# Optimization experiments

Hardware: AMD Instinct MI355X
Metric: run time of the kernel (lower is better)

The kernel has to match this reference:

```python
import jax, jax.numpy as jnp
import numpy as np

N = 50000
E = 800000
NODE_F = 128
LIN = 128
HID = 32
HEADS = 2
OUT = 64
NCLS = 8
NEG_SLOPE = 0.2


def _lin_params(key, fan_in, fan_out, scale=0.05):
    k1, k2 = jax.random.split(key)
    W = jax.random.normal(k1, (fan_in, fan_out), jnp.float32) * scale
    b = jax.random.normal(k2, (fan_out,), jnp.float32) * scale
    return W, b


def setup_inputs() -> dict:
    key = jax.random.key(0)
    ks = jax.random.split(key, 12)
    h = jax.random.normal(ks[0], (N, NODE_F), jnp.float32)
    edge_w = jax.random.uniform(ks[1], (E,), jnp.float32, 1e-3, 1.0)
    src = jax.random.randint(ks[2], (E,), 0, N, jnp.int32)
    dst = jax.random.randint(ks[3], (E,), 0, N, jnp.int32)
    Wn, bn = _lin_params(ks[4], NODE_F, LIN)
    W1s, b1s = _lin_params(ks[5], LIN, HEADS * HID)
    W1d, b1d = _lin_params(ks[6], LIN, HEADS * HID)
    attn1 = jax.random.normal(ks[7], (HEADS, HID), jnp.float32) * 0.05
    W2s, b2s = _lin_params(ks[8], HEADS * HID, OUT)
    W2d, b2d = _lin_params(ks[9], HEADS * HID, OUT)
    attn2 = jax.random.normal(ks[10], (1, OUT), jnp.float32) * 0.05
    k11, k12, k13 = jax.random.split(ks[11], 3)
    Wc1, bc1 = _lin_params(k11, OUT, OUT // 2)
    Wc2, bc2 = _lin_params(k12, OUT // 2, OUT // 4)
    Wcls, bcls = _lin_params(k13, 2 * (OUT // 4), NCLS)
    return dict(h=h, edge_w=edge_w, src=src, dst=dst, Wn=Wn, bn=bn,
                W1s=W1s, b1s=b1s, W1d=W1d, b1d=b1d, attn1=attn1,
                W2s=W2s, b2s=b2s, W2d=W2d, b2d=b2d, attn2=attn2,
                Wc1=Wc1, bc1=bc1, Wc2=Wc2, bc2=bc2, Wcls=Wcls, bcls=bcls)


def _segment_softmax(logits, seg, num_segments):
    # logits: [E, H], seg: [E] destination node ids
    m = jax.ops.segment_max(logits, seg, num_segments=num_segments)
    e = jnp.exp(logits - m[seg])
    s = jax.ops.segment_sum(e, seg, num_segments=num_segments)
    return e / s[seg]


def _gatv2(x, src, dst, Ws, bs, Wd, bd, attn, heads, dim):
    n = x.shape[0]
    fs = (x @ Ws + bs).reshape(n, heads, dim)
    fd = (x @ Wd + bd).reshape(n, heads, dim)
    e = jax.nn.leaky_relu(fs[src] + fd[dst], NEG_SLOPE)  # [E,H,D]
    logits = jnp.einsum('ehd,hd->eh', e, attn)
    alpha = _segment_softmax(logits, dst, n)  # [E,H]
    return jax.ops.segment_sum(fs[src] * alpha[..., None], dst, num_segments=n)


def _forward(h, edge_w, src, dst, Wn, bn, W1s, b1s, W1d, b1d, attn1,
             W2s, b2s, W2d, b2d, attn2, Wc1, bc1, Wc2, bc2, Wcls, bcls):
    n = h.shape[0]
    # EdgeWeightNorm(norm='both'): w / sqrt(out_wdeg(src) * in_wdeg(dst))
    out_wdeg = jax.ops.segment_sum(edge_w, src, num_segments=n)
    in_wdeg = jax.ops.segment_sum(edge_w, dst, num_segments=n)
    norm_w = edge_w * jax.lax.rsqrt(out_wdeg[src]) * jax.lax.rsqrt(in_wdeg[dst])

    node_f = h @ Wn + bn
    # GATv2 layer 1 (dropout is identity in eval)
    g1 = _gatv2(node_f, src, dst, W1s, b1s, W1d, b1d, attn1, HEADS, HID)
    x = jax.nn.elu(g1).reshape(n, HEADS * HID)
    # GATv2 layer 2 (single head)
    g2 = _gatv2(x, src, dst, W2s, b2s, W2d, b2d, attn2, 1, OUT)
    x = jax.nn.elu(g2).reshape(n, OUT)

    # GraphConv norm='none' with edge_weight: sum_in(w * (xW)[src]) + b
    xm = x @ Wc1
    c1 = jax.ops.segment_sum(xm[src] * norm_w[:, None], dst, num_segments=n) + bc1
    x = jax.nn.elu(c1)

    # GraphConv norm='both' (unweighted degrees, clamped to >=1)
    ones_e = jnp.ones((src.shape[0],), x.dtype)
    dout = jnp.clip(jax.ops.segment_sum(ones_e, src, num_segments=n), 1.0)
    din = jnp.clip(jax.ops.segment_sum(ones_e, dst, num_segments=n), 1.0)
    xs = (x @ Wc2) * jax.lax.rsqrt(dout)[:, None]
    c2 = jax.ops.segment_sum(xs[src], dst, num_segments=n) * jax.lax.rsqrt(din)[:, None] + bc2
    x = jax.nn.elu(c2)

    # MLPPredictor: per-edge score from concat(src, dst) features
    score = jnp.concatenate([x[src], x[dst]], axis=1) @ Wcls + bcls
    return score


def reference(h, edge_w, src, dst, Wn, bn, W1s, b1s, W1d, b1d, attn1,
              W2s, b2s, W2d, b2d, attn2, Wc1, bc1, Wc2, bc2, Wcls, bcls):
    return _forward(h, edge_w, src, dst, Wn, bn, W1s, b1s, W1d, b1d, attn1,
                    W2s, b2s, W2d, b2d, attn2, Wc1, bc1, Wc2, bc2, Wcls, bcls)
```

## Files before the change

kernel.cpp:

```cpp
#include <hip/hip_runtime.h>
#include <math.h>

#define NN 50000
#define NE 800000
#define SCAN_BLOCKS ((NN + 255) / 256)

__device__ __forceinline__ float elu1(float x) { return x > 0.f ? x : expm1f(x); }
__device__ __forceinline__ float lrelu(float x) { return x >= 0.f ? x : 0.2f * x; }

__global__ __launch_bounds__(256) void zero_kernel(float* __restrict__ p, int n) {
  int i = blockIdx.x * blockDim.x + threadIdx.x;
  int stride = gridDim.x * blockDim.x;
  for (; i < n; i += stride) p[i] = 0.f;
}

__global__ __launch_bounds__(256) void combine_weights(
    const float* __restrict__ Wn, const float* __restrict__ bn,
    const float* __restrict__ W1s, const float* __restrict__ b1s,
    const float* __restrict__ W1d, const float* __restrict__ b1d,
    float* __restrict__ Wns, float* __restrict__ Wnd,
    float* __restrict__ bns, float* __restrict__ bnd) {
  int t = blockIdx.x * blockDim.x + threadIdx.x;
  if (t < 8192) {
    int i = t >> 6, o = t & 63;
    float acc = 0.f;
    for (int k = 0; k < 128; ++k) acc += Wn[i * 128 + k] * W1s[k * 64 + o];
    Wns[t] = acc;
  } else if (t < 16384) {
    int u = t - 8192;
    int i = u >> 6, o = u & 63;
    float acc = 0.f;
    for (int k = 0; k < 128; ++k) acc += Wn[i * 128 + k] * W1d[k * 64 + o];
    Wnd[u] = acc;
  } else if (t < 16448) {
    int o = t - 16384;
    float acc = b1s[o];
    for (int k = 0; k < 128; ++k) acc += bn[k] * W1s[k * 64 + o];
    bns[o] = acc;
  } else if (t < 16512) {
    int o = t - 16448;
    float acc = b1d[o];
    for (int k = 0; k < 128; ++k) acc += bn[k] * W1d[k * 64 + o];
    bnd[o] = acc;
  }
}

__global__ __launch_bounds__(256) void edge_stats(const float* __restrict__ ew,
                                                  const int* __restrict__ src,
                                                  const int* __restrict__ dst,
                                                  unsigned long long* __restrict__ degw,
                                                  int* __restrict__ cnt) {
  int e = blockIdx.x * blockDim.x + threadIdx.x;
  if (e >= NE) return;
  int s = src[e], d = dst[e];
  unsigned long long pk = (1ULL << 44) | (unsigned long long)(ew[e] * 4294967296.0f);
  atomicAdd(&degw[s], pk);
  atomicAdd(&cnt[d], 1);
}

__global__ __launch_bounds__(256) void decode_degrees(const unsigned long long* __restrict__ degw,
                                                      float* __restrict__ deg) {
  int i = blockIdx.x * blockDim.x + threadIdx.x;
  if (i >= NN) return;
  unsigned long long v = degw[i];
  deg[i] = (float)((double)(v & ((1ULL << 44) - 1)) * (1.0 / 4294967296.0));
  deg[NN + i] = (float)(v >> 44);
}

__global__ __launch_bounds__(256) void csr_block_sums(const int* __restrict__ cnt,
                                                      int* __restrict__ part) {
  __shared__ int sh[256];
  int i = blockIdx.x * 256 + threadIdx.x;
  sh[threadIdx.x] = (i < NN) ? cnt[i] : 0;
  __syncthreads();
  for (int s = 128; s > 0; s >>= 1) {
    if (threadIdx.x < s) sh[threadIdx.x] += sh[threadIdx.x + s];
    __syncthreads();
  }
  if (threadIdx.x == 0) part[blockIdx.x] = sh[0];
}

__global__ __launch_bounds__(256) void csr_scan_part(int* __restrict__ part) {
  __shared__ int sh[256];
  int t = threadIdx.x;
  int v = (t < SCAN_BLOCKS) ? part[t] : 0;
  sh[t] = v;
  __syncthreads();
  for (int off = 1; off < 256; off <<= 1) {
    int add = (t >= off) ? sh[t - off] : 0;
    __syncthreads();
    sh[t] += add;
    __syncthreads();
  }
  if (t < SCAN_BLOCKS) part[t] = sh[t] - v;
}

__global__ __launch_bounds__(256) void csr_scan_write(const int* __restrict__ cnt,
                                                      const int* __restrict__ part,
                                                      int* __restrict__ row_start) {
  __shared__ int sh[256];
  int i = blockIdx.x * 256 + threadIdx.x;
  int t = threadIdx.x;
  int v = (i < NN) ? cnt[i] : 0;
  sh[t] = v;
  __syncthreads();
  for (int off = 1; off < 256; off <<= 1) {
    int add = (t >= off) ? sh[t - off] : 0;
    __syncthreads();
    sh[t] += add;
    __syncthreads();
  }
  if (i < NN) row_start[i] = part[blockIdx.x] + sh[t] - v;
  if (i == 0) row_start[NN] = NE;
}

__global__ __launch_bounds__(256) void csr_fill(const int* __restrict__ src,
                                                const int* __restrict__ dst,
                                                const float* __restrict__ ew,
                                                const int* __restrict__ row_start,
                                                int* __restrict__ fill,
                                                int2* __restrict__ psrcw) {
  int e = blockIdx.x * blockDim.x + threadIdx.x;
  if (e >= NE) return;
  int d = dst[e];
  int pos = row_start[d] + atomicAdd(&fill[d], 1);
  psrcw[pos] = make_int2(src[e], __float_as_int(ew[e]));
}

template <int K, int M, bool ELU_IN, int RS, bool DUAL>
__global__ __launch_bounds__(256) void node_gemm(const float* __restrict__ X,
                                                 const float* __restrict__ W1,
                                                 const float* __restrict__ b1,
                                                 const float* __restrict__ W2,
                                                 const float* __restrict__ b2,
                                                 const float* __restrict__ cnt,
                                                 float* __restrict__ Y1,
                                                 float* __restrict__ Y2) {
  constexpr int RPT = 4;
  constexpr int RG = 256 / M;
  constexpr int ROWS = RG * RPT;
  __shared__ float xs[ROWS][K];
  int row0 = blockIdx.x * ROWS;
  int t = threadIdx.x;
  for (int idx = t; idx < ROWS * K; idx += 256) {
    int r = idx / K, k = idx - r * K;
    int row = row0 + r;
    float v = (row < NN) ? X[row * K + k] : 0.f;
    if (ELU_IN) v = elu1(v);
    xs[r][k] = v;
  }
  __syncthreads();
  int m = t % M, rg = t / M;
  int rbase = rg * RPT;
  float acc1[RPT], acc2[RPT];
#pragma unroll
  for (int j = 0; j < RPT; ++j) {
    acc1[j] = b1 ? b1[m] : 0.f;
    if (DUAL) acc2[j] = b2 ? b2[m] : 0.f;
  }
#pragma unroll 4
  for (int k = 0; k < K; ++k) {
    float w1 = W1[k * M + m];
    float w2 = DUAL ? W2[k * M + m] : 0.f;
#pragma unroll
    for (int j = 0; j < RPT; ++j) {
      float x = xs[rbase + j][k];
      acc1[j] += x * w1;
      if (DUAL) acc2[j] += x * w2;
    }
  }
#pragma unroll
  for (int j = 0; j < RPT; ++j) {
    int row = row0 + rbase + j;
    if (row >= NN) continue;
    float sc = 1.f;
    if (RS == 1) sc = rsqrtf(fmaxf(cnt[row], 1.f));
    if (RS == 2) {
      float wv = cnt[row];
      sc = (wv > 0.f) ? rsqrtf(wv) : 0.f;
    }
    Y1[row * M + m] = acc1[j] * sc;
    if (DUAL) Y2[row * M + m] = acc2[j] * sc;
  }
}

template <int HALFW>
__global__ __launch_bounds__(256) void gat_fused(const int* __restrict__ row_start,
                                                 const int2* __restrict__ psrcw,
                                                 const float* __restrict__ fs,
                                                 const float* __restrict__ fd,
                                                 const float* __restrict__ attn,
                                                 float* __restrict__ g) {
  int n = blockIdx.x * 4 + (threadIdx.x >> 6);
  if (n >= NN) return;
  int lane = threadIdx.x & 63;
  int beg = row_start[n], end = row_start[n + 1];
  float fdv = fd[n * 64 + lane];
  float av = attn[lane];
  float acc = 0.f, den = 0.f;
  int i = beg;
  for (; i + 3 < end; i += 4) {
    int s0 = psrcw[i].x, s1 = psrcw[i + 1].x, s2 = psrcw[i + 2].x, s3 = psrcw[i + 3].x;
    float f0 = fs[s0 * 64 + lane];
    float f1 = fs[s1 * 64 + lane];
    float f2 = fs[s2 * 64 + lane];
    float f3 = fs[s3 * 64 + lane];
    float v0 = lrelu(f0 + fdv) * av;
    float v1 = lrelu(f1 + fdv) * av;
    float v2 = lrelu(f2 + fdv) * av;
    float v3 = lrelu(f3 + fdv) * av;
#pragma unroll
    for (int m = 16; m >= 1; m >>= 1) {
      v0 += __shfl_xor(v0, m, 64);
      v1 += __shfl_xor(v1, m, 64);
      v2 += __shfl_xor(v2, m, 64);
      v3 += __shfl_xor(v3, m, 64);
    }
    if (!HALFW) {
      v0 += __shfl_xor(v0, 32, 64);
      v1 += __shfl_xor(v1, 32, 64);
      v2 += __shfl_xor(v2, 32, 64);
      v3 += __shfl_xor(v3, 32, 64);
    }
    float p0 = __expf(v0);
    float p1 = __expf(v1);
    float p2 = __expf(v2);
    float p3 = __expf(v3);
    acc += f0 * p0 + f1 * p1 + f2 * p2 + f3 * p3;
    den += p0 + p1 + p2 + p3;
  }
  for (; i < end; ++i) {
    int s = psrcw[i].x;
    float fsv = fs[s * 64 + lane];
    float v = lrelu(fsv + fdv) * av;
#pragma unroll
    for (int m = 16; m >= 1; m >>= 1) v += __shfl_xor(v, m, 64);
    if (!HALFW) v += __shfl_xor(v, 32, 64);
    float p = __expf(v);
    acc += fsv * p;
    den += p;
  }
  g[n * 64 + lane] = (end > beg) ? acc / den : 0.f;
}

__global__ __launch_bounds__(256) void gconv1_fused(const int* __restrict__ row_start,
                                                    const int2* __restrict__ psrcw,
                                                    const float* __restrict__ ym,
                                                    const float* __restrict__ bc1,
                                                    float* __restrict__ x3a) {
  int n = blockIdx.x * 4 + (threadIdx.x >> 6);
  if (n >= NN) return;
  int lane = threadIdx.x & 63;
  int half = lane >> 5, f = lane & 31;
  int beg = row_start[n], end = row_start[n + 1];
  float acc = 0.f, wsum = 0.f;
  int i = beg + half;
  for (; i + 2 < end; i += 4) {
    int2 a = psrcw[i], b = psrcw[i + 2];
    float wa = __int_as_float(a.y), wb = __int_as_float(b.y);
    acc += ym[a.x * 32 + f] * wa + ym[b.x * 32 + f] * wb;
    wsum += wa + wb;
  }
  if (i < end) {
    int2 a = psrcw[i];
    float wa = __int_as_float(a.y);
    acc += ym[a.x * 32 + f] * wa;
    wsum += wa;
  }
  acc += __shfl_xor(acc, 32, 64);
  wsum += __shfl_xor(wsum, 32, 64);
  if (lane < 32) {
    float r = (end > beg) ? acc * rsqrtf(wsum) : 0.f;
    x3a[n * 32 + lane] = elu1(r + bc1[lane]);
  }
}

__global__ __launch_bounds__(256) void gconv2_fused(const int* __restrict__ row_start,
                                                    const int2* __restrict__ psrcw,
                                                    const float* __restrict__ xs,
                                                    const float* __restrict__ bc2,
                                                    float* __restrict__ x4) {
  int n = blockIdx.x * 4 + (threadIdx.x >> 6);
  if (n >= NN) return;
  int lane = threadIdx.x & 63;
  int q = lane >> 4, f = lane & 15;
  int beg = row_start[n], end = row_start[n + 1];
  float acc = 0.f;
  int i = beg + q;
  for (; i + 4 < end; i += 8) acc += xs[psrcw[i].x * 16 + f] + xs[psrcw[i + 4].x * 16 + f];
  if (i < end) acc += xs[psrcw[i].x * 16 + f];
  acc += __shfl_xor(acc, 16, 64);
  acc += __shfl_xor(acc, 32, 64);
  if (lane < 16) {
    float len = (float)(end - beg);
    x4[n * 16 + lane] = elu1(acc * rsqrtf(fmaxf(len, 1.f)) + bc2[lane]);
  }
}

__global__ __launch_bounds__(256) void classifier_kernel(const int* __restrict__ src,
                                                         const int* __restrict__ dst,
                                                         const float* __restrict__ x4,
                                                         const float* __restrict__ Wcls,
                                                         const float* __restrict__ bcls,
                                                         float* __restrict__ out) {
  __shared__ float w[256];
  __shared__ float bb[8];
  if (threadIdx.x < 256) w[threadIdx.x] = Wcls[threadIdx.x];
  if (threadIdx.x < 8) bb[threadIdx.x] = bcls[threadIdx.x];
  __syncthreads();
  int t = blockIdx.x * blockDim.x + threadIdx.x;
  int e = t >> 3, c = t & 7;
  if (e >= NE) return;
  int s = src[e], d = dst[e];
  float acc = bb[c];
#pragma unroll
  for (int f = 0; f < 16; ++f) acc += x4[s * 16 + f] * w[f * 8 + c];
#pragma unroll
  for (int f = 0; f < 16; ++f) acc += x4[d * 16 + f] * w[(16 + f) * 8 + c];
  out[e * 8 + c] = acc;
}

extern "C" void kernel_launch(void* const* d_in, const int* in_sizes, int n_in,
                              void* d_out, int out_size, void* d_ws, size_t ws_size,
                              hipStream_t stream) {
  const float* h      = (const float*)d_in[0];
  const float* edge_w = (const float*)d_in[1];
  const int*   src    = (const int*)d_in[2];
  const int*   dst    = (const int*)d_in[3];
  const float* Wn    = (const float*)d_in[4];
  const float* bn    = (const float*)d_in[5];
  const float* W1s   = (const float*)d_in[6];
  const float* b1s   = (const float*)d_in[7];
  const float* W1d   = (const float*)d_in[8];
  const float* b1d   = (const float*)d_in[9];
  const float* attn1 = (const float*)d_in[10];
  const float* W2s   = (const float*)d_in[11];
  const float* b2s   = (const float*)d_in[12];
  const float* W2d   = (const float*)d_in[13];
  const float* b2d   = (const float*)d_in[14];
  const float* attn2 = (const float*)d_in[15];
  const float* Wc1   = (const float*)d_in[16];
  const float* bc1   = (const float*)d_in[17];
  const float* Wc2   = (const float*)d_in[18];
  const float* bc2   = (const float*)d_in[19];
  const float* Wcls  = (const float*)d_in[20];
  const float* bcls  = (const float*)d_in[21];
  float* out = (float*)d_out;

  float* ws = (float*)d_ws;
  size_t off = 0;
  auto alloc = [&](size_t nf) { float* pp = ws + off; off += nf; return pp; };
  float* Wns = alloc(8192);
  float* Wnd = alloc(8192);
  float* bns = alloc(64);
  float* bnd = alloc(64);
  unsigned long long* degw = (unsigned long long*)alloc(2 * NN);
  int*   cnt = (int*)alloc(NN);
  int*   fillp = (int*)alloc(NN);
  float* deg = alloc(2 * NN);
  int*   row_start = (int*)alloc(NN + 1);
  int*   part = (int*)alloc(256);
  int2*  psrcw = (int2*)alloc(2 * NE);
  float* FS  = alloc(64 * NN);
  float* FD  = alloc(64 * NN);
  float* G   = alloc(64 * NN);

  dim3 b256(256);
  const int EB = (NE + 255) / 256;
  const int NB4 = (NN + 3) / 4;

  combine_weights<<<65, b256, 0, stream>>>(Wn, bn, W1s, b1s, W1d, b1d, Wns, Wnd, bns, bnd);

  zero_kernel<<<1024, b256, 0, stream>>>((float*)degw, 4 * NN);
  edge_stats<<<EB, b256, 0, stream>>>(edge_w, src, dst, degw, cnt);
  decode_degrees<<<SCAN_BLOCKS, b256, 0, stream>>>(degw, deg);

  csr_block_sums<<<SCAN_BLOCKS, b256, 0, stream>>>(cnt, part);
  csr_scan_part<<<1, b256, 0, stream>>>(part);
  csr_scan_write<<<SCAN_BLOCKS, b256, 0, stream>>>(cnt, part, row_start);
  csr_fill<<<EB, b256, 0, stream>>>(src, dst, edge_w, row_start, fillp, psrcw);

  node_gemm<128, 64, false, 0, true><<<(NN + 15) / 16, b256, 0, stream>>>(
      h, Wns, bns, Wnd, bnd, nullptr, FS, FD);
  gat_fused<1><<<NB4, b256, 0, stream>>>(row_start, psrcw, FS, FD, attn1, G);

  node_gemm<64, 64, true, 0, true><<<(NN + 15) / 16, b256, 0, stream>>>(
      G, W2s, b2s, W2d, b2d, nullptr, FS, FD);
  gat_fused<0><<<NB4, b256, 0, stream>>>(row_start, psrcw, FS, FD, attn2, G);

  node_gemm<64, 32, true, 2, false><<<(NN + 31) / 32, b256, 0, stream>>>(
      G, Wc1, nullptr, nullptr, nullptr, deg, FS, nullptr);
  gconv1_fused<<<NB4, b256, 0, stream>>>(row_start, psrcw, FS, bc1, FD);

  node_gemm<32, 16, false, 1, false><<<(NN + 63) / 64, b256, 0, stream>>>(
      FD, Wc2, nullptr, nullptr, nullptr, deg + NN, FS, nullptr);
  gconv2_fused<<<NB4, b256, 0, stream>>>(row_start, psrcw, FS, bc2, G);

  classifier_kernel<<<(NE * 8 + 255) / 256, b256, 0, stream>>>(src, dst, G, Wcls, bcls, out);
}
```

Measured before the change: 535.1 us.

## Fuse preprocessing kernels, use rank-based CSR fill, and vectorize classifier

```diff
diff --git a/kernel.cpp b/kernel.cpp
--- a/kernel.cpp
+++ b/kernel.cpp
@@ -3,128 +3,137 @@
 
 #define NN 50000
 #define NE 800000
-#define SCAN_BLOCKS ((NN + 255) / 256)
 
 __device__ __forceinline__ float elu1(float x) { return x > 0.f ? x : expm1f(x); }
 __device__ __forceinline__ float lrelu(float x) { return x >= 0.f ? x : 0.2f * x; }
 
-__global__ __launch_bounds__(256) void zero_kernel(float* __restrict__ p, int n) {
-  int i = blockIdx.x * blockDim.x + threadIdx.x;
-  int stride = gridDim.x * blockDim.x;
-  for (; i < n; i += stride) p[i] = 0.f;
-}
-
-__global__ __launch_bounds__(256) void combine_weights(
+__global__ __launch_bounds__(256) void fat0_kernel(
     const float* __restrict__ Wn, const float* __restrict__ bn,
     const float* __restrict__ W1s, const float* __restrict__ b1s,
     const float* __restrict__ W1d, const float* __restrict__ b1d,
     float* __restrict__ Wns, float* __restrict__ Wnd,
-    float* __restrict__ bns, float* __restrict__ bnd) {
-  int t = blockIdx.x * blockDim.x + threadIdx.x;
-  if (t < 8192) {
-    int i = t >> 6, o = t & 63;
-    float acc = 0.f;
-    for (int k = 0; k < 128; ++k) acc += Wn[i * 128 + k] * W1s[k * 64 + o];
-    Wns[t] = acc;
-  } else if (t < 16384) {
-    int u = t - 8192;
-    int i = u >> 6, o = u & 63;
-    float acc = 0.f;
-    for (int k = 0; k < 128; ++k) acc += Wn[i * 128 + k] * W1d[k * 64 + o];
-    Wnd[u] = acc;
-  } else if (t < 16448) {
-    int o = t - 16384;
-    float acc = b1s[o];
-    for (int k = 0; k < 128; ++k) acc += bn[k] * W1s[k * 64 + o];
-    bns[o] = acc;
-  } else if (t < 16512) {
-    int o = t - 16448;
-    float acc = b1d[o];
-    for (int k = 0; k < 128; ++k) acc += bn[k] * W1d[k * 64 + o];
-    bnd[o] = acc;
-  }
-}
-
-__global__ __launch_bounds__(256) void edge_stats(const float* __restrict__ ew,
-                                                  const int* __restrict__ src,
-                                                  const int* __restrict__ dst,
-                                                  unsigned long long* __restrict__ degw,
-                                                  int* __restrict__ cnt) {
+    float* __restrict__ bns, float* __restrict__ bnd,
+    float* __restrict__ zbase) {
+  if (blockIdx.x < 65) {
+    int t = blockIdx.x * 256 + threadIdx.x;
+    if (t < 8192) {
+      int i = t >> 6, o = t & 63;
+      float acc = 0.f;
+      for (int k = 0; k < 128; ++k) acc += Wn[i * 128 + k] * W1s[k * 64 + o];
+      Wns[t] = acc;
+    } else if (t < 16384) {
+      int u = t - 8192;
+      int i = u >> 6, o = u & 63;
+      float acc = 0.f;
+      for (int k = 0; k < 128; ++k) acc += Wn[i * 128 + k] * W1d[k * 64 + o];
+      Wnd[u] = acc;
+    } else if (t < 16448) {
+      int o = t - 16384;
+      float acc = b1s[o];
+      for (int k = 0; k < 128; ++k) acc += bn[k] * W1s[k * 64 + o];
+      bns[o] = acc;
+    } else if (t < 16512) {
+      int o = t - 16448;
+      float acc = b1d[o];
+      for (int k = 0; k < 128; ++k) acc += bn[k] * W1d[k * 64 + o];
+      bnd[o] = acc;
+    }
+  } else {
+    int i = (blockIdx.x - 65) * 256 + threadIdx.x;
+    if (i < 3 * NN) zbase[i] = 0.f;
+  }
+}
+
+__global__ __launch_bounds__(256) void edge_rank(const int* __restrict__ dst,
+                                                 int* __restrict__ cnt,
+                                                 int* __restrict__ rank) {
   int e = blockIdx.x * blockDim.x + threadIdx.x;
   if (e >= NE) return;
-  int s = src[e], d = dst[e];
-  unsigned long long pk = (1ULL << 44) | (unsigned long long)(ew[e] * 4294967296.0f);
-  atomicAdd(&degw[s], pk);
-  atomicAdd(&cnt[d], 1);
-}
-
-__global__ __launch_bounds__(256) void decode_degrees(const unsigned long long* __restrict__ degw,
-                                                      float* __restrict__ deg) {
-  int i = blockIdx.x * blockDim.x + threadIdx.x;
-  if (i >= NN) return;
-  unsigned long long v = degw[i];
-  deg[i] = (float)((double)(v & ((1ULL << 44) - 1)) * (1.0 / 4294967296.0));
-  deg[NN + i] = (float)(v >> 44);
-}
-
-__global__ __launch_bounds__(256) void csr_block_sums(const int* __restrict__ cnt,
-                                                      int* __restrict__ part) {
-  __shared__ int sh[256];
-  int i = blockIdx.x * 256 + threadIdx.x;
-  sh[threadIdx.x] = (i < NN) ? cnt[i] : 0;
+  rank[e] = atomicAdd(&cnt[dst[e]], 1);
+}
+
+__global__ __launch_bounds__(1024) void scan_all(const int* __restrict__ cnt,
+                                                 int* __restrict__ row_start) {
+  __shared__ int sh[1024];
+  int t = threadIdx.x;
+  const int CHUNK = (NN + 1023) / 1024;
+  int base = t * CHUNK;
+  int lim = base + CHUNK;
+  if (lim > NN) lim = NN;
+  int s = 0;
+#pragma unroll 8
+  for (int i = base; i < lim; ++i) s += cnt[i];
+  sh[t] = s;
   __syncthreads();
-  for (int s = 128; s > 0; s >>= 1) {
-    if (threadIdx.x < s) sh[threadIdx.x] += sh[threadIdx.x + s];
-    __syncthreads();
-  }
-  if (threadIdx.x == 0) part[blockIdx.x] = sh[0];
-}
-
-__global__ __launch_bounds__(256) void csr_scan_part(int* __restrict__ part) {
-  __shared__ int sh[256];
-  int t = threadIdx.x;
-  int v = (t < SCAN_BLOCKS) ? part[t] : 0;
-  sh[t] = v;
-  __syncthreads();
-  for (int off = 1; off < 256; off <<= 1) {
+  for (int off = 1; off < 1024; off <<= 1) {
     int add = (t >= off) ? sh[t - off] : 0;
     __syncthreads();
     sh[t] += add;
     __syncthreads();
   }
-  if (t < SCAN_BLOCKS) part[t] = sh[t] - v;
-}
-
-__global__ __launch_bounds__(256) void csr_scan_write(const int* __restrict__ cnt,
-                                                      const int* __restrict__ part,
-                                                      int* __restrict__ row_start) {
-  __shared__ int sh[256];
-  int i = blockIdx.x * 256 + threadIdx.x;
+  int run = sh[t] - s;
+#pragma unroll 8
+  for (int i = base; i < lim; ++i) {
+    row_start[i] = run;
+    run += cnt[i];
+  }
+  if (base < NN && base + CHUNK >= NN) row_start[NN] = run;
+}
+
+template <int K, int M, bool ELU_IN, int RS, bool DUAL>
+__device__ __forceinline__ void gemm_body(int blk, float* __restrict__ xs,
+                                          const float* __restrict__ X,
+                                          const float* __restrict__ W1,
+                                          const float* __restrict__ b1,
+                                          const float* __restrict__ W2,
+                                          const float* __restrict__ b2,
+                                          const float* __restrict__ cnt,
+                                          float* __restrict__ Y1,
+                                          float* __restrict__ Y2) {
+  constexpr int RPT = 4;
+  constexpr int ROWS = (256 / M) * RPT;
+  int row0 = blk * ROWS;
   int t = threadIdx.x;
-  int v = (i < NN) ? cnt[i] : 0;
-  sh[t] = v;
+  for (int idx = t; idx < ROWS * K; idx += 256) {
+    int r = idx / K, k = idx - r * K;
+    int row = row0 + r;
+    float v = (row < NN) ? X[row * K + k] : 0.f;
+    if (ELU_IN) v = elu1(v);
+    xs[r * K + k] = v;
+  }
   __syncthreads();
-  for (int off = 1; off < 256; off <<= 1) {
-    int add = (t >= off) ? sh[t - off] : 0;
-    __syncthreads();
-    sh[t] += add;
-    __syncthreads();
-  }
-  if (i < NN) row_start[i] = part[blockIdx.x] + sh[t] - v;
-  if (i == 0) row_start[NN] = NE;
-}
-
-__global__ __launch_bounds__(256) void csr_fill(const int* __restrict__ src,
-                                                const int* __restrict__ dst,
-                                                const float* __restrict__ ew,
-                                                const int* __restrict__ row_start,
-                                                int* __restrict__ fill,
-                                                int2* __restrict__ psrcw) {
-  int e = blockIdx.x * blockDim.x + threadIdx.x;
-  if (e >= NE) return;
-  int d = dst[e];
-  int pos = row_start[d] + atomicAdd(&fill[d], 1);
-  psrcw[pos] = make_int2(src[e], __float_as_int(ew[e]));
+  int m = t % M, rg = t / M;
+  int rbase = rg * RPT;
+  float acc1[RPT], acc2[RPT];
+#pragma unroll
+  for (int j = 0; j < RPT; ++j) {
+    acc1[j] = b1 ? b1[m] : 0.f;
+    if (DUAL) acc2[j] = b2 ? b2[m] : 0.f;
+  }
+#pragma unroll 4
+  for (int k = 0; k < K; ++k) {
+    float w1 = W1[k * M + m];
+    float w2 = DUAL ? W2[k * M + m] : 0.f;
+#pragma unroll
+    for (int j = 0; j < RPT; ++j) {
+      float x = xs[(rbase + j) * K + k];
+      acc1[j] += x * w1;
+      if (DUAL) acc2[j] += x * w2;
+    }
+  }
+#pragma unroll
+  for (int j = 0; j < RPT; ++j) {
+    int row = row0 + rbase + j;
+    if (row >= NN) continue;
+    float sc = 1.f;
+    if (RS == 1) sc = rsqrtf(fmaxf(cnt[row], 1.f));
+    if (RS == 2) {
+      float wv = cnt[row];
+      sc = (wv > 0.f) ? rsqrtf(wv) : 0.f;
+    }
+    Y1[row * M + m] = acc1[j] * sc;
+    if (DUAL) Y2[row * M + m] = acc2[j] * sc;
+  }
 }
 
 template <int K, int M, bool ELU_IN, int RS, bool DUAL>
@@ -136,51 +145,47 @@
                                                  const float* __restrict__ cnt,
                                                  float* __restrict__ Y1,
                                                  float* __restrict__ Y2) {
-  constexpr int RPT = 4;
-  constexpr int RG = 256 / M;
-  constexpr int ROWS = RG * RPT;
-  __shared__ float xs[ROWS][K];
-  int row0 = blockIdx.x * ROWS;
-  int t = threadIdx.x;
-  for (int idx = t; idx < ROWS * K; idx += 256) {
-    int r = idx / K, k = idx - r * K;
-    int row = row0 + r;
-    float v = (row < NN) ? X[row * K + k] : 0.f;
-    if (ELU_IN) v = elu1(v);
-    xs[r][k] = v;
-  }
-  __syncthreads();
-  int m = t % M, rg = t / M;
-  int rbase = rg * RPT;
-  float acc1[RPT], acc2[RPT];
-#pragma unroll
-  for (int j = 0; j < RPT; ++j) {
-    acc1[j] = b1 ? b1[m] : 0.f;
-    if (DUAL) acc2[j] = b2 ? b2[m] : 0.f;
-  }
-#pragma unroll 4
-  for (int k = 0; k < K; ++k) {
-    float w1 = W1[k * M + m];
-    float w2 = DUAL ? W2[k * M + m] : 0.f;
-#pragma unroll
-    for (int j = 0; j < RPT; ++j) {
-      float x = xs[rbase + j][k];
-      acc1[j] += x * w1;
-      if (DUAL) acc2[j] += x * w2;
-    }
-  }
-#pragma unroll
-  for (int j = 0; j < RPT; ++j) {
-    int row = row0 + rbase + j;
-    if (row >= NN) continue;
-    float sc = 1.f;
-    if (RS == 1) sc = rsqrtf(fmaxf(cnt[row], 1.f));
-    if (RS == 2) {
-      float wv = cnt[row];
-      sc = (wv > 0.f) ? rsqrtf(wv) : 0.f;
-    }
-    Y1[row * M + m] = acc1[j] * sc;
-    if (DUAL) Y2[row * M + m] = acc2[j] * sc;
+  __shared__ float xs[(256 / M) * 4 * K];
+  gemm_body<K, M, ELU_IN, RS, DUAL>(blockIdx.x, xs, X, W1, b1, W2, b2, cnt, Y1, Y2);
+}
+
+__global__ __launch_bounds__(256) void fatB_kernel(
+    const int* __restrict__ src, const int* __restrict__ dst,
+    const float* __restrict__ ew, const int* __restrict__ row_start,
+    const int* __restrict__ rank, int2* __restrict__ psrcw,
+    unsigned long long* __restrict__ degw,
+    const float* __restrict__ h, const float* __restrict__ Wns,
+    const float* __restrict__ bns, const float* __restrict__ Wnd,
+    const float* __restrict__ bnd, float* __restrict__ FS, float* __restrict__ FD) {
+  __shared__ float xs[16 * 128];
+  int c = blockIdx.x >> 1;
+  if (blockIdx.x & 1) {
+    gemm_body<128, 64, false, 0, true>(c, xs, h, Wns, bns, Wnd, bnd, nullptr, FS, FD);
+  } else {
+    int e = c * 256 + threadIdx.x;
+    if (e >= NE) return;
+    int s = src[e], d = dst[e];
+    float w = ew[e];
+    psrcw[row_start[d] + rank[e]] = make_int2(s, __float_as_int(w));
+    unsigned long long pk = (1ULL << 44) | (unsigned long long)(w * 4294967296.0f);
+    atomicAdd(&degw[s], pk);
+  }
+}
+
+__global__ __launch_bounds__(256) void fatL2_kernel(
+    const float* __restrict__ G, const float* __restrict__ W2s,
+    const float* __restrict__ b2s, const float* __restrict__ W2d,
+    const float* __restrict__ b2d, float* __restrict__ FS, float* __restrict__ FD,
+    const unsigned long long* __restrict__ degw, float* __restrict__ deg) {
+  __shared__ float xs[16 * 64];
+  if (blockIdx.x < 3125) {
+    gemm_body<64, 64, true, 0, true>(blockIdx.x, xs, G, W2s, b2s, W2d, b2d, nullptr, FS, FD);
+  } else {
+    int i = (blockIdx.x - 3125) * 256 + threadIdx.x;
+    if (i >= NN) return;
+    unsigned long long v = degw[i];
+    deg[i] = (float)((double)(v & ((1ULL << 44) - 1)) * (1.0 / 4294967296.0));
+    deg[NN + i] = (float)(v >> 44);
   }
 }
 
@@ -309,15 +314,39 @@
   if (threadIdx.x < 8) bb[threadIdx.x] = bcls[threadIdx.x];
   __syncthreads();
   int t = blockIdx.x * blockDim.x + threadIdx.x;
-  int e = t >> 3, c = t & 7;
+  int e = t >> 1, c0 = (t & 1) * 4;
   if (e >= NE) return;
   int s = src[e], d = dst[e];
-  float acc = bb[c];
-#pragma unroll
-  for (int f = 0; f < 16; ++f) acc += x4[s * 16 + f] * w[f * 8 + c];
-#pragma unroll
-  for (int f = 0; f < 16; ++f) acc += x4[d * 16 + f] * w[(16 + f) * 8 + c];
-  out[e * 8 + c] = acc;
+  const float4* xsv = (const float4*)&x4[s * 16];
+  const float4* xdv = (const float4*)&x4[d * 16];
+  float acc0 = bb[c0], acc1 = bb[c0 + 1], acc2 = bb[c0 + 2], acc3 = bb[c0 + 3];
+#pragma unroll
+  for (int q = 0; q < 4; ++q) {
+    float4 xv = xsv[q];
+#pragma unroll
+    for (int j = 0; j < 4; ++j) {
+      float x = j == 0 ? xv.x : j == 1 ? xv.y : j == 2 ? xv.z : xv.w;
+      const float* wr = &w[(q * 4 + j) * 8 + c0];
+      acc0 += x * wr[0];
+      acc1 += x * wr[1];
+      acc2 += x * wr[2];
+      acc3 += x * wr[3];
+    }
+  }
+#pragma unroll
+  for (int q = 0; q < 4; ++q) {
+    float4 xv = xdv[q];
+#pragma unroll
+    for (int j = 0; j < 4; ++j) {
+      float x = j == 0 ? xv.x : j == 1 ? xv.y : j == 2 ? xv.z : xv.w;
+      const float* wr = &w[(16 + q * 4 + j) * 8 + c0];
+      acc0 += x * wr[0];
+      acc1 += x * wr[1];
+      acc2 += x * wr[2];
+      acc3 += x * wr[3];
+    }
+  }
+  *(float4*)&out[e * 8 + c0] = make_float4(acc0, acc1, acc2, acc3);
 }
 
 extern "C" void kernel_launch(void* const* d_in, const int* in_sizes, int n_in,
@@ -349,52 +378,40 @@
 
   float* ws = (float*)d_ws;
   size_t off = 0;
-  auto alloc = [&](size_t nf) { float* pp = ws + off; off += nf; return pp; };
+  auto alloc = [&](size_t nf) { float* pp = ws + off; off += (nf + 3) & ~(size_t)3; return pp; };
   float* Wns = alloc(8192);
   float* Wnd = alloc(8192);
   float* bns = alloc(64);
   float* bnd = alloc(64);
   unsigned long long* degw = (unsigned long long*)alloc(2 * NN);
   int*   cnt = (int*)alloc(NN);
-  int*   fillp = (int*)alloc(NN);
   float* deg = alloc(2 * NN);
   int*   row_start = (int*)alloc(NN + 1);
-  int*   part = (int*)alloc(256);
   int2*  psrcw = (int2*)alloc(2 * NE);
   float* FS  = alloc(64 * NN);
   float* FD  = alloc(64 * NN);
   float* G   = alloc(64 * NN);
+  int*   rank = (int*)G;
 
   dim3 b256(256);
   const int EB = (NE + 255) / 256;
   const int NB4 = (NN + 3) / 4;
 
-  combine_weights<<<65, b256, 0, stream>>>(Wn, bn, W1s, b1s, W1d, b1d, Wns, Wnd, bns, bnd);
-
-  zero_kernel<<<1024, b256, 0, stream>>>((float*)degw, 4 * NN);
-  edge_stats<<<EB, b256, 0, stream>>>(edge_w, src, dst, degw, cnt);
-  decode_degrees<<<SCAN_BLOCKS, b256, 0, stream>>>(degw, deg);
-
-  csr_block_sums<<<SCAN_BLOCKS, b256, 0, stream>>>(cnt, part);
-  csr_scan_part<<<1, b256, 0, stream>>>(part);
-  csr_scan_write<<<SCAN_BLOCKS, b256, 0, stream>>>(cnt, part, row_start);
-  csr_fill<<<EB, b256, 0, stream>>>(src, dst, edge_w, row_start, fillp, psrcw);
-
-  node_gemm<128, 64, false, 0, true><<<(NN + 15) / 16, b256, 0, stream>>>(
-      h, Wns, bns, Wnd, bnd, nullptr, FS, FD);
+  fat0_kernel<<<65 + (3 * NN + 255) / 256, b256, 0, stream>>>(
+      Wn, bn, W1s, b1s, W1d, b1d, Wns, Wnd, bns, bnd, (float*)degw);
+  edge_rank<<<EB, b256, 0, stream>>>(dst, cnt, rank);
+  scan_all<<<1, 1024, 0, stream>>>(cnt, row_start);
+  fatB_kernel<<<2 * EB, b256, 0, stream>>>(src, dst, edge_w, row_start, rank, psrcw,
+                                           degw, h, Wns, bns, Wnd, bnd, FS, FD);
   gat_fused<1><<<NB4, b256, 0, stream>>>(row_start, psrcw, FS, FD, attn1, G);
-
-  node_gemm<64, 64, true, 0, true><<<(NN + 15) / 16, b256, 0, stream>>>(
-      G, W2s, b2s, W2d, b2d, nullptr, FS, FD);
+  fatL2_kernel<<<3125 + (NN + 255) / 256, b256, 0, stream>>>(G, W2s, b2s, W2d, b2d,
+                                                             FS, FD, degw, deg);
   gat_fused<0><<<NB4, b256, 0, stream>>>(row_start, psrcw, FS, FD, attn2, G);
-
   node_gemm<64, 32, true, 2, false><<<(NN + 31) / 32, b256, 0, stream>>>(
       G, Wc1, nullptr, nullptr, nullptr, deg, FS, nullptr);
   gconv1_fused<<<NB4, b256, 0, stream>>>(row_start, psrcw, FS, bc1, FD);
-
   node_gemm<32, 16, false, 1, false><<<(NN + 63) / 64, b256, 0, stream>>>(
       FD, Wc2, nullptr, nullptr, nullptr, deg + NN, FS, nullptr);
   gconv2_fused<<<NB4, b256, 0, stream>>>(row_start, psrcw, FS, bc2, G);
-
-  classifier_kernel<<<(NE * 8 + 255) / 256, b256, 0, stream>>>(src, dst, G, Wcls, bcls, out);
-}
+  classifier_kernel<<<(NE * 2 + 255) / 256, b256, 0, stream>>>(src, dst, G, Wcls, bcls, out);
+}
```

After: 491.1 us. 8.2% less time.
